# Performance work log

Hardware: AMD Instinct MI355X
Metric: run time of the kernel (lower is better)

## Reference

```python
import math
import jax, jax.numpy as jnp
import numpy as np

PHI = (1.0 + math.sqrt(5.0)) / 2.0
B, S, E, H, L = 2, 2048, 1024, 16, 5
DH = E // H


def setup_inputs() -> dict:
    key = jax.random.key(0)
    ks = jax.random.split(key, 16)
    rn = lambda k, sh, sc=0.02: jax.random.normal(k, sh, jnp.float32) * sc
    return {
        'x': jax.random.normal(ks[0], (B, S, E), jnp.float32),
        'consciousness_levels': jax.random.uniform(ks[1], (B, H), jnp.float32),
        'Wc': rn(ks[2], (L, E, E)), 'bc': jnp.zeros((L, E), jnp.float32),
        'Wf': rn(ks[3], (L, E, H)), 'bf': jnp.zeros((L, H), jnp.float32),
        'Wq': rn(ks[4], (E, E)), 'bq': jnp.zeros((E,), jnp.float32),
        'Wk': rn(ks[5], (E, E)), 'bk': jnp.zeros((E,), jnp.float32),
        'Wv': rn(ks[6], (E, E)), 'bv': jnp.zeros((E,), jnp.float32),
        'Wo': rn(ks[7], (E, E)), 'bo': jnp.zeros((E,), jnp.float32),
        'Wc1': rn(ks[8], (2 * DH, E)), 'bc1': jnp.zeros((E,), jnp.float32),
        'Wc2': rn(ks[9], (E, 1)), 'bc2': jnp.zeros((1,), jnp.float32),
        'gate': jax.random.normal(ks[10], (L, H), jnp.float32) / math.sqrt(H),
        'phi_phase': PHI * jnp.arange(H, dtype=jnp.float32),
        'ln_g': jnp.ones((E,), jnp.float32), 'ln_b': jnp.zeros((E,), jnp.float32),
    }


def reference(x, consciousness_levels, Wc, bc, Wf, bf, Wq, bq, Wk, bk, Wv, bv,
              Wo, bo, Wc1, bc1, Wc2, bc2, gate, phi_phase, ln_g, ln_b):
    b, s, e = x.shape
    l, _, h = Wf.shape
    dh = e // h
    # per-level consciousness scalar: consciousness_levels[:, level % num_heads] -> [B, L]
    cl = consciousness_levels[:, jnp.arange(l) % h]
    # consciousness-enhanced features: mean over L of (x @ Wc_l + bc_l) * cl[:, l]
    feat = jnp.einsum('bse,leo->lbso', x, Wc) + bc[:, None, None, :]   # [L,B,S,E]
    ce = jnp.mean(feat * cl.T[:, :, None, None], axis=0)                # [B,S,E]
    # QKV projections (spectral_norm linears; normalized weights supplied directly)
    Q = (ce @ Wq + bq).reshape(b, s, h, dh).transpose(0, 2, 1, 3)       # [B,H,S,Dh]
    K = (ce @ Wk + bk).reshape(b, s, h, dh).transpose(0, 2, 1, 3)
    V = (ce @ Wv + bv).reshape(b, s, h, dh).transpose(0, 2, 1, 3)
    scores = jnp.einsum('bhsd,bhtd->bhst', Q, K) / math.sqrt(dh)        # [B,H,S,S]
    # phi-harmonic phase modulation (scalar per (B,H), averaged over levels)
    pooled = ce.mean(axis=1)                                            # [B,E]
    freq = jnp.einsum('be,leh->lbh', pooled, Wf) + bf[:, None, :]       # [L,B,H]
    phase = jnp.sin(phi_phase[None, None, :] * freq * cl.T[:, :, None]).mean(axis=0)  # [B,H]
    scores = scores + 0.1 * phase[:, :, None, None]
    # quantum coherence gate per (B,H): sigmoid MLP on pooled Q/K head features
    ci = jnp.concatenate([Q.mean(axis=2), K.mean(axis=2)], axis=-1)     # [B,H,2*Dh]
    cw = jax.nn.sigmoid(jax.nn.gelu(ci @ Wc1 + bc1, approximate=False) @ Wc2 + bc2)  # [B,H,1]
    scores = scores * (1.0 + cw[..., None])
    aw = jax.nn.softmax(scores, axis=-1)
    # consciousness gating on attention weights, then re-softmax
    gw = jax.nn.softmax(gate, axis=1)                                   # [L,H]
    factor = jnp.prod(1.0 + 0.1 * cl[:, :, None] * gw[None, :, :], axis=1)  # [B,H]
    aw = jax.nn.softmax(aw * factor[:, :, None, None], axis=-1)
    attended = jnp.einsum('bhst,bhtd->bhsd', aw, V)
    out = attended.transpose(0, 2, 1, 3).reshape(b, s, e) @ Wo + bo
    y = x + out  # dropout is identity in eval
    mu = y.mean(axis=-1, keepdims=True)
    var = ((y - mu) ** 2).mean(axis=-1, keepdims=True)
    return (y - mu) / jnp.sqrt(var + 1e-5) * ln_g + ln_b
```

## Files before the change

### kernel.cpp

```cpp
#include <hip/hip_runtime.h>
#include <math.h>

#define BB 2
#define SS 2048
#define EE 1024
#define HH 16
#define LL 5
#define DH 64
#define QS (3 * 1024)

typedef __attribute__((ext_vector_type(8))) short bf16x8;
typedef __attribute__((ext_vector_type(4))) float f32x4;

__device__ __forceinline__ unsigned short f2bf(float f) {
  unsigned u = __float_as_uint(f);
  u += 0x7fffu + ((u >> 16) & 1u);
  return (unsigned short)(u >> 16);
}
__device__ __forceinline__ float bf2f(unsigned short u) {
  return __uint_as_float((unsigned)u << 16);
}
__device__ __forceinline__ f32x4 mfma16(bf16x8 a, bf16x8 b, f32x4 c) {
  return __builtin_amdgcn_mfma_f32_16x16x32_bf16(a, b, c, 0, 0, 0);
}
__device__ __forceinline__ unsigned cvtpk(float a, float b) {
  unsigned r;
  asm("v_cvt_pk_bf16_f32 %0, %1, %2" : "=v"(r) : "v"(a), "v"(b));
  return r;
}
__device__ __forceinline__ void gload16(const unsigned short* g, unsigned short* l) {
  __builtin_amdgcn_global_load_lds(
      (const __attribute__((address_space(1))) void*)g,
      (__attribute__((address_space(3))) void*)l, 16, 0, 0);
}

__global__ void prep_pack(const float* __restrict__ cons, const float* __restrict__ gate,
                          const float* __restrict__ bc,
                          const float* __restrict__ bq, const float* __restrict__ bk,
                          const float* __restrict__ bv,
                          float* __restrict__ beff, float* __restrict__ bqkv,
                          float* __restrict__ factor) {
  int i = blockIdx.x * 256 + threadIdx.x;
  if (i == 0) {
    float gw[LL][HH];
    for (int l = 0; l < LL; ++l) {
      float mx = -1e30f;
      for (int h = 0; h < HH; ++h) mx = fmaxf(mx, gate[l * HH + h]);
      float s = 0.f;
      for (int h = 0; h < HH; ++h) { gw[l][h] = expf(gate[l * HH + h] - mx); s += gw[l][h]; }
      for (int h = 0; h < HH; ++h) gw[l][h] /= s;
    }
    for (int b = 0; b < BB; ++b)
      for (int h = 0; h < HH; ++h) {
        float f = 1.f;
        for (int l = 0; l < LL; ++l) f *= 1.f + 0.1f * cons[b * HH + l] * gw[l][h];
        factor[b * HH + h] = f;
      }
  }
  if (i < BB * EE) {
    int b = i >> 10, e = i & 1023;
    float a = 0.f;
    #pragma unroll
    for (int l = 0; l < LL; ++l) a += cons[b * HH + l] * bc[l * EE + e];
    beff[i] = a * (1.f / LL);
  } else {
    int j = i - BB * EE;
    float v = (j < EE) ? bq[j] : (j < 2 * EE) ? bk[j - EE] : bv[j - 2 * EE];
    bqkv[j] = v;
  }
}

__global__ __launch_bounds__(256) void wceffT_kernel(const float* __restrict__ Wc,
                                                     const float* __restrict__ cons,
                                                     unsigned short* __restrict__ Wt) {
  int o0 = blockIdx.x * 64, e0 = blockIdx.y * 64, b = blockIdx.z;
  __shared__ float t[64][69];
  int tid = threadIdx.x;
  float w[LL];
  #pragma unroll
  for (int l = 0; l < LL; ++l) w[l] = cons[b * HH + l] * (1.f / LL);
  #pragma unroll
  for (int i = 0; i < 4; ++i) {
    int idx = tid + i * 256;
    int r = idx >> 4, c4 = idx & 15;
    float4 acc = {0.f, 0.f, 0.f, 0.f};
    #pragma unroll
    for (int l = 0; l < LL; ++l) {
      float4 v = *(const float4*)&Wc[(long)l * EE * EE + (long)(e0 + r) * EE + o0 + c4 * 4];
      acc.x += w[l] * v.x; acc.y += w[l] * v.y; acc.z += w[l] * v.z; acc.w += w[l] * v.w;
    }
    t[r][c4 * 4 + 0] = acc.x; t[r][c4 * 4 + 1] = acc.y;
    t[r][c4 * 4 + 2] = acc.z; t[r][c4 * 4 + 3] = acc.w;
  }
  __syncthreads();
  #pragma unroll
  for (int i = 0; i < 2; ++i) {
    int idx = tid + i * 256;
    int o = idx >> 3, ech = idx & 7;
    unsigned short u[8];
    #pragma unroll
    for (int j = 0; j < 8; ++j) u[j] = f2bf(t[ech * 8 + j][o]);
    unsigned short* dst = Wt + (long)b * EE * EE + (long)(o0 + o) * EE + e0 + ech * 8;
    *(ushort4*)&dst[0] = *(ushort4*)&u[0];
    *(ushort4*)&dst[4] = *(ushort4*)&u[4];
  }
}

__global__ __launch_bounds__(256) void wT4_kernel(
    const float* __restrict__ W0, const float* __restrict__ W1,
    const float* __restrict__ W2, const float* __restrict__ W3,
    unsigned short* __restrict__ Wqkvt, unsigned short* __restrict__ Wot) {
  int z = blockIdx.z;
  const float* W = (z == 0) ? W0 : (z == 1) ? W1 : (z == 2) ? W2 : W3;
  unsigned short* Wt = (z < 3) ? (Wqkvt + (size_t)z * EE * EE) : Wot;
  int o0 = blockIdx.x * 64, e0 = blockIdx.y * 64;
  __shared__ float t[64][69];
  int tid = threadIdx.x;
  #pragma unroll
  for (int i = 0; i < 4; ++i) {
    int idx = tid + i * 256;
    int r = idx >> 4, c4 = idx & 15;
    float4 v = *(const float4*)&W[(long)(e0 + r) * EE + o0 + c4 * 4];
    t[r][c4 * 4 + 0] = v.x; t[r][c4 * 4 + 1] = v.y;
    t[r][c4 * 4 + 2] = v.z; t[r][c4 * 4 + 3] = v.w;
  }
  __syncthreads();
  #pragma unroll
  for (int i = 0; i < 2; ++i) {
    int idx = tid + i * 256;
    int o = idx >> 3, ech = idx & 7;
    unsigned short u[8];
    #pragma unroll
    for (int j = 0; j < 8; ++j) u[j] = f2bf(t[ech * 8 + j][o]);
    unsigned short* dst = Wt + (long)(o0 + o) * EE + e0 + ech * 8;
    *(ushort4*)&dst[0] = *(ushort4*)&u[0];
    *(ushort4*)&dst[4] = *(ushort4*)&u[4];
  }
}

__global__ void cvt_bf_kernel(const float* __restrict__ in, unsigned short* __restrict__ out) {
  long i = (long)blockIdx.x * 256 + threadIdx.x;
  float4 a = ((const float4*)in)[i * 2];
  float4 b = ((const float4*)in)[i * 2 + 1];
  ushort4 u0 = make_ushort4(f2bf(a.x), f2bf(a.y), f2bf(a.z), f2bf(a.w));
  ushort4 u1 = make_ushort4(f2bf(b.x), f2bf(b.y), f2bf(b.z), f2bf(b.w));
  ((ushort4*)out)[i * 2] = u0;
  ((ushort4*)out)[i * 2 + 1] = u1;
}

template <int OUTBF>
__global__ __launch_bounds__(256) void gemm128(
    const unsigned short* __restrict__ A, const unsigned short* __restrict__ Bt,
    const float* __restrict__ bias, void* __restrict__ C,
    int N, int K, long As_z, long Ws_z, long Bs_z, long Cs_z) {
  int flat = blockIdx.x + gridDim.x * (blockIdx.y + gridDim.y * blockIdx.z);
  int nwg = gridDim.x * gridDim.y * gridDim.z;
  flat = (flat & 7) * (nwg >> 3) + (flat >> 3);
  int nt_ = flat % gridDim.x;
  int rest = flat / gridDim.x;
  int mt_ = rest % gridDim.y;
  int z = rest / gridDim.y;

  const unsigned short* Ab = A + z * As_z + (long)mt_ * 128 * K;
  const unsigned short* Bb = Bt + z * Ws_z + (long)nt_ * 128 * K;
  const float* bb = bias + z * Bs_z + nt_ * 128;

  __shared__ __align__(16) unsigned short As[2][128 * 64];
  __shared__ __align__(16) unsigned short Bs[2][128 * 64];
  int tid = threadIdx.x;
  int w = tid >> 6, lane = tid & 63, c = lane & 15, g = lane >> 4;
  int wrow = (w >> 1) * 64, wcol = (w & 1) * 64;

  #define STG128(srcp, dstbuf, kt)                                             \
    {                                                                          \
      const unsigned short* s_ = (srcp) + (kt) * 64;                           \
      _Pragma("unroll") for (int j = 0; j < 4; ++j) {                          \
        int idx = tid + j * 256;                                               \
        int row = idx >> 3, ch = idx & 7;                                      \
        gload16(s_ + (long)row * K + ((ch ^ (row & 7)) << 3),                  \
                &dstbuf[(idx & ~63) * 8 + (lane)*8]);                          \
      }                                                                        \
    }

  f32x4 acc[4][4];
  #pragma unroll
  for (int mi = 0; mi < 4; ++mi)
    #pragma unroll
    for (int ni = 0; ni < 4; ++ni) acc[mi][ni] = {0.f, 0.f, 0.f, 0.f};

  int nk = K >> 6;
  STG128(Ab, As[0], 0) STG128(Bb, Bs[0], 0)
  __syncthreads();
  int buf = 0;
  for (int kt = 0; kt < nk; ++kt) {
    if (kt + 1 < nk) { STG128(Ab, As[buf ^ 1], kt + 1) STG128(Bb, Bs[buf ^ 1], kt + 1) }
    #pragma unroll
    for (int kk = 0; kk < 2; ++kk) {
      bf16x8 af[4], bfv[4];
      #pragma unroll
      for (int mi = 0; mi < 4; ++mi) {
        int row = wrow + mi * 16 + c;
        af[mi] = *(const bf16x8*)&As[buf][row * 64 + ((((kk << 2) + g) ^ (row & 7)) << 3)];
      }
      #pragma unroll
      for (int ni = 0; ni < 4; ++ni) {
        int row = wcol + ni * 16 + c;
        bfv[ni] = *(const bf16x8*)&Bs[buf][row * 64 + ((((kk << 2) + g) ^ (row & 7)) << 3)];
      }
      #pragma unroll
      for (int mi = 0; mi < 4; ++mi)
        #pragma unroll
        for (int ni = 0; ni < 4; ++ni)
          acc[mi][ni] = mfma16(af[mi], bfv[ni], acc[mi][ni]);
    }
    __syncthreads();
    buf ^= 1;
  }

  float bval[4];
  #pragma unroll
  for (int ni = 0; ni < 4; ++ni) bval[ni] = bb[wcol + ni * 16 + c];
  #pragma unroll
  for (int mi = 0; mi < 4; ++mi)
    #pragma unroll
    for (int ni = 0; ni < 4; ++ni) {
      long col = (long)nt_ * 128 + wcol + ni * 16 + c;
      #pragma unroll
      for (int r = 0; r < 4; ++r) {
        long row = (long)mt_ * 128 + wrow + mi * 16 + g * 4 + r;
        float v = acc[mi][ni][r] + bval[ni];
        if (OUTBF)
          ((unsigned short*)C)[z * Cs_z + row * N + col] = f2bf(v);
        else
          ((float*)C)[z * Cs_z + row * N + col] = v;
      }
    }
  #undef STG128
}

__global__ void mean2_kernel(const unsigned short* __restrict__ QKVb,
                             float* __restrict__ Qm, float* __restrict__ Km) {
  int z = blockIdx.z;
  const unsigned short* in = QKVb + z * EE;
  float* out = z ? Km : Qm;
  int e = blockIdx.x * 256 + threadIdx.x;
  int b = e >> 10, ee = e & 1023;
  int s0 = blockIdx.y * 128;
  const unsigned short* p = in + ((long)b * SS + s0) * QS + ee;
  float acc = 0.f;
  for (int i = 0; i < 128; ++i) acc += bf2f(p[(long)i * QS]);
  atomicAdd(&out[e], acc * (1.f / SS));
}

__global__ __launch_bounds__(256) void cw_kernel(
    const float* __restrict__ Qm, const float* __restrict__ Km,
    const float* __restrict__ Wc1, const float* __restrict__ bc1,
    const float* __restrict__ Wc2, const float* __restrict__ bc2,
    float* __restrict__ alpha) {
  int bh = blockIdx.x, b = bh / HH, h = bh % HH;
  __shared__ float ci[128];
  __shared__ float pr[4];
  int tid = threadIdx.x;
  if (tid < 64) ci[tid] = Qm[b * EE + h * DH + tid];
  else if (tid < 128) ci[tid] = Km[b * EE + h * DH + (tid - 64)];
  __syncthreads();
  float part = 0.f;
  for (int j = tid; j < EE; j += 256) {
    float acc = bc1[j];
    #pragma unroll 8
    for (int i = 0; i < 128; ++i) acc += ci[i] * Wc1[i * EE + j];
    float ge = 0.5f * acc * (1.f + erff(acc * 0.70710678118654752f));
    part += ge * Wc2[j];
  }
  #pragma unroll
  for (int off = 32; off; off >>= 1) part += __shfl_xor(part, off);
  if ((tid & 63) == 0) pr[tid >> 6] = part;
  __syncthreads();
  if (tid == 0) {
    float tot = pr[0] + pr[1] + pr[2] + pr[3] + bc2[0];
    float cw = 1.f / (1.f + expf(-tot));
    alpha[bh] = 1.f + cw;
  }
}

__global__ __launch_bounds__(256) void repack_vT(const unsigned short* __restrict__ Vh,
                                                 unsigned short* __restrict__ Vt,
                                                 float* __restrict__ Vsum) {
  int st = blockIdx.x, h = blockIdx.y, b = blockIdx.z;
  __shared__ unsigned short tile[64][66];
  int tid = threadIdx.x;
  const unsigned short* src = Vh + ((long)(b * SS) + st * 64) * QS + h * 64;
  #pragma unroll
  for (int i = 0; i < 2; ++i) {
    int idx = tid + i * 256;
    int s = idx >> 3, ch = idx & 7;
    #pragma unroll
    for (int j = 0; j < 8; ++j) tile[s][ch * 8 + j] = src[(long)s * QS + ch * 8 + j];
  }
  __syncthreads();
  unsigned short* dst = Vt + ((long)(b * HH + h) * 64) * SS + st * 64;
  #pragma unroll
  for (int i = 0; i < 2; ++i) {
    int idx = tid + i * 256;
    int d = idx >> 3, sch = idx & 7;
    unsigned short u[8];
    #pragma unroll
    for (int j = 0; j < 8; ++j) u[j] = tile[sch * 8 + j][d];
    *(ushort4*)&dst[(long)d * SS + sch * 8] = *(ushort4*)&u[0];
    *(ushort4*)&dst[(long)d * SS + sch * 8 + 4] = *(ushort4*)&u[4];
  }
  {
    int d = tid & 63, quarter = tid >> 6;
    float part = 0.f;
    #pragma unroll
    for (int j = 0; j < 16; ++j) part += bf2f(tile[quarter * 16 + j][d]);
    atomicAdd(&Vsum[((long)(b * HH + h)) * 64 + d], part);
  }
}

__global__ __launch_bounds__(256, 4) void attn_lin(
    const unsigned short* __restrict__ QKV,
    const unsigned short* __restrict__ Vt,
    const float* __restrict__ alpha,
    float* __restrict__ Np0, float* __restrict__ Np1,
    float* __restrict__ m1p) {
  int flat = blockIdx.x;
  flat = (flat & 7) * 128 + (flat >> 3);
  int qt = flat & 15, h = (flat >> 4) & 15, b = (flat >> 8) & 1, part = flat >> 9;
  int bh = b * HH + h;
  int tid = threadIdx.x;
  int l = tid & 63, w = tid >> 6, c = l & 15, g = l >> 4;
  __shared__ __align__(16) unsigned short kbuf[2][4096];
  __shared__ __align__(16) unsigned short vbuf[2][4096];
  __shared__ __align__(16) unsigned short pws[4][1024];

  const unsigned short* Kb_ =
      QKV + (long)b * SS * QS + EE + h * 64 + (long)part * 1024 * QS;
  const unsigned short* Vb_ = Vt + (long)bh * 64 * SS + part * 1024;
  float* Np = part ? Np1 : Np0;
  const float scaleE = alpha[bh] * 0.125f;
  const f32x4 zero4 = {0.f, 0.f, 0.f, 0.f};

  bf16x8 qf[2][2];
  {
    const unsigned short* qp =
        QKV + ((long)b * SS + qt * 128 + w * 32 + c) * QS + h * 64;
    qf[0][0] = *(const bf16x8*)(qp + 8 * g);
    qf[0][1] = *(const bf16x8*)(qp + 32 + 8 * g);
    qf[1][0] = *(const bf16x8*)(qp + 16 * QS + 8 * g);
    qf[1][1] = *(const bf16x8*)(qp + 16 * QS + 32 + 8 * g);
  }

  int off1 = tid, off2 = tid + 256;
  int r1 = off1 >> 3, ch1 = ((off1 & 7) ^ (r1 & 7)) << 3;
  int r2 = off2 >> 3, ch2 = ((off2 & 7) ^ (r2 & 7)) << 3;
  const unsigned short* kg1 = Kb_ + (long)r1 * QS + ch1;
  const unsigned short* kg2 = Kb_ + (long)r2 * QS + ch2;
  const unsigned short* vg1 = Vb_ + (long)r1 * SS + ch1;
  const unsigned short* vg2 = Vb_ + (long)r2 * SS + ch2;

  gload16(kg1, &kbuf[0][off1 * 8]);
  gload16(kg2, &kbuf[0][off2 * 8]);
  gload16(vg1, &vbuf[0][off1 * 8]);
  gload16(vg2, &vbuf[0][off2 * 8]);
  kg1 += (long)64 * QS; kg2 += (long)64 * QS; vg1 += 64; vg2 += 64;
  __syncthreads();

  f32x4 N1[4][2];
  #pragma unroll
  for (int d = 0; d < 4; ++d) { N1[d][0] = zero4; N1[d][1] = zero4; }
  float m1l0 = 0.f, m1l1 = 0.f;
  unsigned short* pw = pws[w];

  int buf = 0;
  const int NT2 = 16;
  for (int t = 0; t < NT2; ++t) {
    if (t + 1 < NT2) {
      gload16(kg1, &kbuf[buf ^ 1][off1 * 8]);
      gload16(kg2, &kbuf[buf ^ 1][off2 * 8]);
      gload16(vg1, &vbuf[buf ^ 1][off1 * 8]);
      gload16(vg2, &vbuf[buf ^ 1][off2 * 8]);
      kg1 += (long)64 * QS; kg2 += (long)64 * QS; vg1 += 64; vg2 += 64;
    }
    const unsigned short* kb = kbuf[buf];
    const unsigned short* vb = vbuf[buf];
    __builtin_amdgcn_s_setprio(1);
    #pragma unroll
    for (int half = 0; half < 2; ++half) {
      #pragma unroll
      for (int mth = 0; mth < 2; ++mth) {
        int mt = half * 2 + mth;
        int r = mt * 16 + c;
        bf16x8 a0 = *(const bf16x8*)&kb[r * 64 + ((g ^ (r & 7)) << 3)];
        bf16x8 a1 = *(const bf16x8*)&kb[r * 64 + (((4 + g) ^ (r & 7)) << 3)];
        int ch = 2 * mth + (g >> 1);
        #pragma unroll
        for (int qb = 0; qb < 2; ++qb) {
          f32x4 s = mfma16(a0, qf[qb][0], zero4);
          s = mfma16(a1, qf[qb][1], s);
          float u0 = __expf(s[0] * scaleE), u1 = __expf(s[1] * scaleE);
          float u2 = __expf(s[2] * scaleE), u3 = __expf(s[3] * scaleE);
          if (qb == 0) m1l0 += (u0 + u1) + (u2 + u3);
          else         m1l1 += (u0 + u1) + (u2 + u3);
          int row = qb * 16 + c;
          int swz = (ch ^ (row & 3) ^ ((row >> 2) & 3)) & 3;
          *(uint2*)&pw[row * 32 + (swz << 3) + ((g & 1) << 2)] =
              make_uint2(cvtpk(u0, u1), cvtpk(u2, u3));
        }
      }
      bf16x8 pf[2];
      #pragma unroll
      for (int qb = 0; qb < 2; ++qb) {
        int row = qb * 16 + c;
        int swz = (g ^ (row & 3) ^ ((row >> 2) & 3)) & 3;
        pf[qb] = *(const bf16x8*)&pw[row * 32 + (swz << 3)];
      }
      #pragma unroll
      for (int dblk = 0; dblk < 4; ++dblk) {
        int r = dblk * 16 + c;
        bf16x8 v = *(const bf16x8*)&vb[r * 64 + (((half * 4 + g) ^ (r & 7)) << 3)];
        N1[dblk][0] = mfma16(v, pf[0], N1[dblk][0]);
        N1[dblk][1] = mfma16(v, pf[1], N1[dblk][1]);
      }
    }
    __builtin_amdgcn_s_setprio(0);
    __syncthreads();
    buf ^= 1;
  }

  m1l0 += __shfl_xor(m1l0, 16); m1l0 += __shfl_xor(m1l0, 32);
  m1l1 += __shfl_xor(m1l1, 16); m1l1 += __shfl_xor(m1l1, 32);
  if (l < 16) {
    long mb = ((long)(part * BB + b) * HH + h) * SS + qt * 128 + w * 32;
    m1p[mb + c] = m1l0;
    m1p[mb + 16 + c] = m1l1;
  }

  #pragma unroll
  for (int qb = 0; qb < 2; ++qb) {
    float* np = Np + ((long)b * SS + qt * 128 + w * 32 + qb * 16 + c) * EE + h * 64;
    #pragma unroll
    for (int dblk = 0; dblk < 4; ++dblk) {
      float4 o = {N1[dblk][qb][0], N1[dblk][qb][1], N1[dblk][qb][2], N1[dblk][qb][3]};
      *(float4*)&np[dblk * 16 + 4 * g] = o;
    }
  }
}

__global__ __launch_bounds__(256) void attn_combine(
    const float* __restrict__ Np0, const float* __restrict__ Np1,
    const float* __restrict__ m1p, const float* __restrict__ Vsum,
    const float* __restrict__ factor, unsigned short* __restrict__ att) {
  int row = blockIdx.x;
  int b = row >> 11, s = row & 2047;
  int e0 = threadIdx.x * 4;
  int h = e0 >> 6, d = e0 & 63;
  int bh = b * HH + h;
  float m1 = m1p[((long)b * HH + h) * SS + s] +
             m1p[((long)(BB + b) * HH + h) * SS + s];
  float fac = factor[bh];
  float c1 = fac / m1;
  float invden = 1.f / ((float)SS + fac);
  long base = (long)row * EE + e0;
  float4 n0 = *(const float4*)&Np0[base];
  float4 n1 = *(const float4*)&Np1[base];
  float4 vs = *(const float4*)&Vsum[bh * 64 + d];
  float o0 = (vs.x + c1 * (n0.x + n1.x)) * invden;
  float o1 = (vs.y + c1 * (n0.y + n1.y)) * invden;
  float o2 = (vs.z + c1 * (n0.z + n1.z)) * invden;
  float o3 = (vs.w + c1 * (n0.w + n1.w)) * invden;
  *(uint2*)&att[base] = make_uint2(cvtpk(o0, o1), cvtpk(o2, o3));
}

__global__ __launch_bounds__(256) void ln_kernel(
    const float* __restrict__ x, const float* __restrict__ proj,
    const float* __restrict__ g, const float* __restrict__ bb,
    float* __restrict__ out) {
  long row = blockIdx.x;
  const float* xp = x + row * EE;
  const float* pp = proj + row * EE;
  int tid = threadIdx.x;
  float v[4];
  float s = 0.f;
  __shared__ float r1[4], r2[4];
  #pragma unroll
  for (int i = 0; i < 4; ++i) {
    int e = tid + i * 256;
    v[i] = xp[e] + pp[e];
    s += v[i];
  }
  #pragma unroll
  for (int off = 32; off; off >>= 1) s += __shfl_xor(s, off);
  if ((tid & 63) == 0) r1[tid >> 6] = s;
  __syncthreads();
  float mean = (r1[0] + r1[1] + r1[2] + r1[3]) * (1.f / EE);
  float s2 = 0.f;
  #pragma unroll
  for (int i = 0; i < 4; ++i) { float d = v[i] - mean; s2 += d * d; }
  #pragma unroll
  for (int off = 32; off; off >>= 1) s2 += __shfl_xor(s2, off);
  if ((tid & 63) == 0) r2[tid >> 6] = s2;
  __syncthreads();
  float rstd = rsqrtf((r2[0] + r2[1] + r2[2] + r2[3]) * (1.f / EE) + 1e-5f);
  #pragma unroll
  for (int i = 0; i < 4; ++i) {
    int e = tid + i * 256;
    out[row * EE + e] = (v[i] - mean) * rstd * g[e] + bb[e];
  }
}

extern "C" void kernel_launch(void* const* d_in, const int* in_sizes, int n_in,
                              void* d_out, int out_size, void* d_ws, size_t ws_size,
                              hipStream_t stream) {
  (void)in_sizes; (void)n_in; (void)out_size; (void)ws_size;
  const float* x    = (const float*)d_in[0];
  const float* cons = (const float*)d_in[1];
  const float* Wc   = (const float*)d_in[2];
  const float* bc   = (const float*)d_in[3];
  const float* Wq   = (const float*)d_in[6];
  const float* bq   = (const float*)d_in[7];
  const float* Wk   = (const float*)d_in[8];
  const float* bk   = (const float*)d_in[9];
  const float* Wv   = (const float*)d_in[10];
  const float* bv   = (const float*)d_in[11];
  const float* Wo   = (const float*)d_in[12];
  const float* bo   = (const float*)d_in[13];
  const float* Wc1  = (const float*)d_in[14];
  const float* bc1  = (const float*)d_in[15];
  const float* Wc2  = (const float*)d_in[16];
  const float* bc2  = (const float*)d_in[17];
  const float* gate = (const float*)d_in[18];
  const float* ln_g = (const float*)d_in[20];
  const float* ln_b = (const float*)d_in[21];
  float* out = (float*)d_out;

  const size_t MSZ = (size_t)BB * SS * EE;
  float* p = (float*)d_ws;
  float* beff = p;  p += BB * EE;
  float* factor = p; p += 32;
  float* alpha  = p; p += 32;
  float* Qm   = p;  p += BB * EE;
  float* Km   = p;  p += BB * EE;
  float* Vsum = p;  p += BB * EE;
  float* bqkv = p;  p += QS;
  float* proj = p;  p += MSZ;
  unsigned short* q = (unsigned short*)p;
  unsigned short* xbf  = q;  q += MSZ;
  unsigned short* cebf = q;  q += MSZ;
  unsigned short* QKVb = q;  q += 3 * MSZ;
  unsigned short* Vt   = q;  q += MSZ;
  unsigned short* attb = q;  q += MSZ;
  unsigned short* Weft = q;  q += (size_t)BB * EE * EE;
  unsigned short* Wqkvt= q;  q += (size_t)3 * EE * EE;
  unsigned short* Wot  = q;  q += (size_t)EE * EE;
  float* m1p = (float*)q;    q += 2 * 2 * BB * HH * SS;
  float* Np0 = (float*)xbf;
  float* Np1 = proj;

  prep_pack<<<(BB * EE + QS) / 256, 256, 0, stream>>>(cons, gate, bc, bq, bk, bv,
                                                      beff, bqkv, factor);
  wceffT_kernel<<<dim3(16, 16, 2), 256, 0, stream>>>(Wc, cons, Weft);
  wT4_kernel<<<dim3(16, 16, 4), 256, 0, stream>>>(Wq, Wk, Wv, Wo, Wqkvt, Wot);
  cvt_bf_kernel<<<MSZ / 8 / 256, 256, 0, stream>>>(x, xbf);

  dim3 cgrid(EE / 128, SS / 128, BB);
  gemm128<1><<<cgrid, 256, 0, stream>>>(xbf, Weft, beff, cebf, EE, EE,
                                        (long)SS * EE, (long)EE * EE, EE, (long)SS * EE);
  dim3 qgrid(QS / 128, SS / 128, BB);
  gemm128<1><<<qgrid, 256, 0, stream>>>(cebf, Wqkvt, bqkv, QKVb, QS, EE,
                                        (long)SS * EE, 0, 0, (long)SS * QS);

  hipMemsetAsync(Qm, 0, (size_t)3 * BB * EE * sizeof(float), stream);
  mean2_kernel<<<dim3((BB * EE) / 256, SS / 128, 2), 256, 0, stream>>>(QKVb, Qm, Km);
  cw_kernel<<<BB * HH, 256, 0, stream>>>(Qm, Km, Wc1, bc1, Wc2, bc2, alpha);

  repack_vT<<<dim3(SS / 64, HH, BB), 256, 0, stream>>>(QKVb + 2 * EE, Vt, Vsum);

  attn_lin<<<1024, 256, 0, stream>>>(QKVb, Vt, alpha, Np0, Np1, m1p);
  attn_combine<<<BB * SS, 256, 0, stream>>>(Np0, Np1, m1p, Vsum, factor, attb);

  gemm128<0><<<cgrid, 256, 0, stream>>>(attb, Wot, bo, proj, EE, EE,
                                        (long)SS * EE, 0, 0, (long)SS * EE);
  ln_kernel<<<BB * SS, 256, 0, stream>>>(x, proj, ln_g, ln_b, out);
}
```

Baseline: 216.9 us.

## Load V fragments directly to registers and fold score scale into Q

The attention kernel stops staging V tiles through double-buffered LDS and instead loads each lane's V fragments straight from global memory into registers at the start of every tile iteration. It also pre-multiplies the Q fragments by the softmax scale once, in bf16, so the per-score multiply before exp is removed. This cuts LDS footprint and LDS traffic, which could raise occupancy. The trade-offs are exposed global-load latency with no prefetch, extra VGPR pressure, and a small precision change from rounding the scaled Q to bf16.

Result: slower. 247.9 us (+14.3%).

```diff
diff --git a/kernel.cpp b/kernel.cpp
--- a/kernel.cpp
+++ b/kernel.cpp
@@ -27,6 +27,17 @@
   unsigned r;
   asm("v_cvt_pk_bf16_f32 %0, %1, %2" : "=v"(r) : "v"(a), "v"(b));
   return r;
+}
+__device__ __forceinline__ bf16x8 scale8(bf16x8 v, float s) {
+  union { bf16x8 h; unsigned u[4]; } in, out;
+  in.h = v;
+  #pragma unroll
+  for (int j = 0; j < 4; ++j) {
+    float lo = bf2f((unsigned short)(in.u[j] & 0xffffu));
+    float hi = bf2f((unsigned short)(in.u[j] >> 16));
+    out.u[j] = cvtpk(lo * s, hi * s);
+  }
+  return out.h;
 }
 __device__ __forceinline__ void gload16(const unsigned short* g, unsigned short* l) {
   __builtin_amdgcn_global_load_lds(
@@ -331,7 +342,6 @@
   int tid = threadIdx.x;
   int l = tid & 63, w = tid >> 6, c = l & 15, g = l >> 4;
   __shared__ __align__(16) unsigned short kbuf[2][4096];
-  __shared__ __align__(16) unsigned short vbuf[2][4096];
   __shared__ __align__(16) unsigned short pws[4][1024];
 
   const unsigned short* Kb_ =
@@ -345,10 +355,10 @@
   {
     const unsigned short* qp =
         QKV + ((long)b * SS + qt * 128 + w * 32 + c) * QS + h * 64;
-    qf[0][0] = *(const bf16x8*)(qp + 8 * g);
-    qf[0][1] = *(const bf16x8*)(qp + 32 + 8 * g);
-    qf[1][0] = *(const bf16x8*)(qp + 16 * QS + 8 * g);
-    qf[1][1] = *(const bf16x8*)(qp + 16 * QS + 32 + 8 * g);
+    qf[0][0] = scale8(*(const bf16x8*)(qp + 8 * g), scaleE);
+    qf[0][1] = scale8(*(const bf16x8*)(qp + 32 + 8 * g), scaleE);
+    qf[1][0] = scale8(*(const bf16x8*)(qp + 16 * QS + 8 * g), scaleE);
+    qf[1][1] = scale8(*(const bf16x8*)(qp + 16 * QS + 32 + 8 * g), scaleE);
   }
 
   int off1 = tid, off2 = tid + 256;
@@ -356,14 +366,10 @@
   int r2 = off2 >> 3, ch2 = ((off2 & 7) ^ (r2 & 7)) << 3;
   const unsigned short* kg1 = Kb_ + (long)r1 * QS + ch1;
   const unsigned short* kg2 = Kb_ + (long)r2 * QS + ch2;
-  const unsigned short* vg1 = Vb_ + (long)r1 * SS + ch1;
-  const unsigned short* vg2 = Vb_ + (long)r2 * SS + ch2;
 
   gload16(kg1, &kbuf[0][off1 * 8]);
   gload16(kg2, &kbuf[0][off2 * 8]);
-  gload16(vg1, &vbuf[0][off1 * 8]);
-  gload16(vg2, &vbuf[0][off2 * 8]);
-  kg1 += (long)64 * QS; kg2 += (long)64 * QS; vg1 += 64; vg2 += 64;
+  kg1 += (long)64 * QS; kg2 += (long)64 * QS;
   __syncthreads();
 
   f32x4 N1[4][2];
@@ -375,15 +381,19 @@
   int buf = 0;
   const int NT2 = 16;
   for (int t = 0; t < NT2; ++t) {
+    bf16x8 vr[2][4];
+    #pragma unroll
+    for (int half = 0; half < 2; ++half)
+      #pragma unroll
+      for (int dblk = 0; dblk < 4; ++dblk)
+        vr[half][dblk] = *(const bf16x8*)(Vb_ + (long)(dblk * 16 + c) * SS +
+                                          t * 64 + ((half * 4 + g) << 3));
     if (t + 1 < NT2) {
       gload16(kg1, &kbuf[buf ^ 1][off1 * 8]);
       gload16(kg2, &kbuf[buf ^ 1][off2 * 8]);
-      gload16(vg1, &vbuf[buf ^ 1][off1 * 8]);
-      gload16(vg2, &vbuf[buf ^ 1][off2 * 8]);
-      kg1 += (long)64 * QS; kg2 += (long)64 * QS; vg1 += 64; vg2 += 64;
+      kg1 += (long)64 * QS; kg2 += (long)64 * QS;
     }
     const unsigned short* kb = kbuf[buf];
-    const unsigned short* vb = vbuf[buf];
     __builtin_amdgcn_s_setprio(1);
     #pragma unroll
     for (int half = 0; half < 2; ++half) {
@@ -398,8 +408,8 @@
         for (int qb = 0; qb < 2; ++qb) {
           f32x4 s = mfma16(a0, qf[qb][0], zero4);
           s = mfma16(a1, qf[qb][1], s);
-          float u0 = __expf(s[0] * scaleE), u1 = __expf(s[1] * scaleE);
-          float u2 = __expf(s[2] * scaleE), u3 = __expf(s[3] * scaleE);
+          float u0 = __expf(s[0]), u1 = __expf(s[1]);
+          float u2 = __expf(s[2]), u3 = __expf(s[3]);
           if (qb == 0) m1l0 += (u0 + u1) + (u2 + u3);
           else         m1l1 += (u0 + u1) + (u2 + u3);
           int row = qb * 16 + c;
@@ -417,10 +427,8 @@
       }
       #pragma unroll
       for (int dblk = 0; dblk < 4; ++dblk) {
-        int r = dblk * 16 + c;
-        bf16x8 v = *(const bf16x8*)&vb[r * 64 + (((half * 4 + g) ^ (r & 7)) << 3)];
-        N1[dblk][0] = mfma16(v, pf[0], N1[dblk][0]);
-        N1[dblk][1] = mfma16(v, pf[1], N1[dblk][1]);
+        N1[dblk][0] = mfma16(vr[half][dblk], pf[0], N1[dblk][0]);
+        N1[dblk][1] = mfma16(vr[half][dblk], pf[1], N1[dblk][1]);
       }
     }
     __builtin_amdgcn_s_setprio(0);
```
